# Optimization experiments

Hardware: AMD Instinct MI355X
Metric: run time of the kernel (lower is better)

Reference implementation:

```python
import jax, jax.numpy as jnp
import numpy as np


def setup_inputs() -> dict:
    key = jax.random.key(0)
    k0, k1, k2, k3 = jax.random.split(key, 4)
    B, T, C = 4, 2048, 1024
    x = jax.random.normal(k0, (B, T, C), dtype=jnp.float32)
    s = C ** -0.5  # init-scale for weights so activations stay O(1)
    Wq = jax.random.normal(k1, (C, C), dtype=jnp.float32) * s
    Wk = jax.random.normal(k2, (C, C), dtype=jnp.float32) * s
    Wv = jax.random.normal(k3, (C, C), dtype=jnp.float32) * s
    return {"x": x, "Wq": Wq, "Wk": Wk, "Wv": Wv}


def reference(x, Wq, Wk, Wv):
    B, T, C = x.shape
    # torch nn.Linear: y = x @ W.T
    q = jnp.einsum('btc,dc->btd', x, Wq)
    k = jnp.einsum('btc,dc->btd', x, Wk)
    v = jnp.einsum('btc,dc->btd', x, Wv)
    scale = C ** -0.5
    wei = jnp.einsum('btd,bsd->bts', q, k) * scale  # [B, T, T]
    causal = jnp.tril(jnp.ones((T, T), dtype=bool))
    wei = jnp.where(causal, wei, -jnp.inf)
    wei = jax.nn.softmax(wei, axis=-1)
    out = jnp.einsum('bts,bsd->btd', wei, v)
    return out
```

## Files before the change

### kernel.cpp

```cpp
#include <hip/hip_runtime.h>
#include <hip/hip_bf16.h>
#include <math.h>

#define B_ 4
#define T_ 2048
#define C_ 1024
#define M_ (B_*T_)

typedef __attribute__((ext_vector_type(8))) __bf16 bf16x8;
typedef __attribute__((ext_vector_type(4))) float floatx4;

__device__ inline float bf2f(unsigned short u){
    return __uint_as_float(((unsigned)u) << 16);
}
__device__ inline unsigned short f2bf(float f){
    unsigned u = __float_as_uint(f);
    unsigned r = (u + 0x7fffu + ((u >> 16) & 1u)) >> 16;
    return (unsigned short)r;
}

__device__ inline void llds16(const unsigned short* g, unsigned short* lds){
    __builtin_amdgcn_global_load_lds(
        (const __attribute__((address_space(1))) unsigned int*)g,
        (__attribute__((address_space(3))) unsigned int*)(unsigned int)(uintptr_t)lds,
        16, 0, 0);
}

#define NX_ (M_*C_/4)
#define NW_ (C_*C_/4)
__global__ __launch_bounds__(256) void cast_all(
    const float* __restrict__ x, const float* __restrict__ wq,
    const float* __restrict__ wk, const float* __restrict__ wv,
    unsigned short* __restrict__ xb, unsigned short* __restrict__ wb)
{
    int i = blockIdx.x * 256 + threadIdx.x;
    const float* src; unsigned short* dst; int idx;
    if (i < NX_){ src = x; dst = xb; idx = i; }
    else {
        i -= NX_;
        int w = i / NW_; idx = i - w * NW_;
        src = (w == 0) ? wq : ((w == 1) ? wk : wv);
        dst = wb + (size_t)w * C_ * C_;
    }
    float4 v = ((const float4*)src)[idx];
    ((ushort4*)dst)[idx] = make_ushort4(f2bf(v.x), f2bf(v.y), f2bf(v.z), f2bf(v.w));
}

template<int WM, int WN>
__device__ inline void gemm_core(const unsigned short* __restrict__ A,
                                 const unsigned short* __restrict__ Bm,
                                 int lda, int ldb, int m0, int n0, int kTiles,
                                 unsigned short* As, unsigned short* Bs,
                                 floatx4 (*acc)[WN/16])
{
    const int tid  = threadIdx.x;
    const int lane = tid & 63;
    const int wave = tid >> 6;
    const int wm = (wave >> 1) * WM;
    const int wn = (wave & 1) * WN;
    const int fr = lane & 15;
    const int fq = lane >> 4;
    const int cxor = fr & 7;
    const int sr = lane >> 3;
    const int sc = ((lane & 7) ^ ((lane >> 3) & 7)) * 8;

    const unsigned short* gA = A  + (size_t)(m0 + wave * (WM/2) + sr) * lda + sc;
    const unsigned short* gB = Bm + (size_t)(n0 + wave * (WN/2) + sr) * ldb + sc;
    unsigned short* ldsA = As + wave * (WM/2) * 64;
    unsigned short* ldsB = Bs + wave * (WN/2) * 64;

    for (int kt = 0; kt < kTiles; kt++){
        const int k0 = kt * 64;
        __syncthreads();
        #pragma unroll
        for (int i = 0; i < WM/16; i++)
            llds16(gA + (size_t)(i * 8) * lda + k0, ldsA + i * 8 * 64);
        #pragma unroll
        for (int i = 0; i < WN/16; i++)
            llds16(gB + (size_t)(i * 8) * ldb + k0, ldsB + i * 8 * 64);
        __syncthreads();
        #pragma unroll
        for (int ks = 0; ks < 64; ks += 32){
            const int cpos = (((ks >> 3) + fq) ^ cxor) * 8;
            bf16x8 af[WM/16], bv[WN/16];
            #pragma unroll
            for (int i = 0; i < WM/16; i++)
                af[i] = *(const bf16x8*)(As + (wm + i*16 + fr) * 64 + cpos);
            #pragma unroll
            for (int j = 0; j < WN/16; j++)
                bv[j] = *(const bf16x8*)(Bs + (wn + j*16 + fr) * 64 + cpos);
            #pragma unroll
            for (int i = 0; i < WM/16; i++)
                #pragma unroll
                for (int j = 0; j < WN/16; j++)
                    acc[i][j] = __builtin_amdgcn_mfma_f32_16x16x32_bf16(af[i], bv[j], acc[i][j], 0, 0, 0);
        }
    }
}

__global__ __launch_bounds__(256, 4) void proj_gemm(
    const unsigned short* __restrict__ xb,
    const unsigned short* __restrict__ Wb,
    unsigned short* __restrict__ Qb, unsigned short* __restrict__ Kb,
    unsigned short* __restrict__ Vt)
{
    __shared__ unsigned short As[128 * 64];
    __shared__ unsigned short Bs[128 * 64];
    const int L = blockIdx.x;
    const int k = L & 7, j = L >> 3;
    const int m0 = (k * 8 + (j & 7)) * 128;
    const int n0 = ((j >> 3) & 7) * 128;
    const int z  = j >> 6;
    const unsigned short* W = Wb + (size_t)z * C_ * C_;

    floatx4 acc[4][4];
    #pragma unroll
    for (int i = 0; i < 4; i++)
        #pragma unroll
        for (int jj = 0; jj < 4; jj++) acc[i][jj] = (floatx4){0.f,0.f,0.f,0.f};
    gemm_core<64, 64>(xb, W, C_, C_, m0, n0, C_ / 64, As, Bs, acc);

    const int lane = threadIdx.x & 63, wave = threadIdx.x >> 6;
    const int wm = (wave >> 1) * 64, wn = (wave & 1) * 64;
    const int fr = lane & 15, fq = lane >> 4;

    if (z < 2){
        unsigned short* Y = z ? Kb : Qb;
        #pragma unroll
        for (int i = 0; i < 4; i++)
            #pragma unroll
            for (int jj = 0; jj < 4; jj++)
                #pragma unroll
                for (int r = 0; r < 4; r++){
                    int row = m0 + wm + i*16 + fq*4 + r;
                    int col = n0 + wn + jj*16 + fr;
                    Y[(size_t)row * C_ + col] = f2bf(acc[i][jj][r]);
                }
    } else {
        #pragma unroll
        for (int i = 0; i < 4; i++)
            #pragma unroll
            for (int jj = 0; jj < 4; jj++){
                int row = m0 + wm + i*16 + fq*4;
                int col = n0 + wn + jj*16 + fr;
                int b = row / T_, t = row % T_;
                ushort4 o = make_ushort4(f2bf(acc[i][jj][0]), f2bf(acc[i][jj][1]),
                                         f2bf(acc[i][jj][2]), f2bf(acc[i][jj][3]));
                *(ushort4*)&Vt[(size_t)b * C_ * T_ + (size_t)col * T_ + t] = o;
            }
    }
}

__global__ __launch_bounds__(256, 4) void score_gemm(
    const unsigned short* __restrict__ Qb, const unsigned short* __restrict__ Kb,
    unsigned short* __restrict__ P, float* __restrict__ l)
{
    const int L = blockIdx.x;
    const int k = L & 7, j = L >> 3;
    const int b = j / 17, rr = j % 17;
    int ti, si;
    if (rr <= 15 - k){ ti = 15 - k; si = rr; }
    else             { ti = k;      si = rr - (16 - k); }
    const int t0 = ti * 128, s0 = si * 128;

    __shared__ unsigned short As[128 * 64];
    __shared__ unsigned short Bs[128 * 64];
    floatx4 acc[4][4];
    #pragma unroll
    for (int i = 0; i < 4; i++)
        #pragma unroll
        for (int jj = 0; jj < 4; jj++) acc[i][jj] = (floatx4){0.f,0.f,0.f,0.f};
    gemm_core<64, 64>(Qb + (size_t)b * T_ * C_, Kb + (size_t)b * T_ * C_,
                      C_, C_, t0, s0, C_ / 64, As, Bs, acc);

    const int lane = threadIdx.x & 63, wave = threadIdx.x >> 6;
    const int wm = (wave >> 1) * 64, wn = (wave & 1) * 64;
    const int fr = lane & 15, fq = lane >> 4;
    unsigned short* Pb = P + (size_t)b * T_ * T_;
    const float scale = 0.03125f;
    float rsl[4][4];
    #pragma unroll
    for (int i = 0; i < 4; i++)
        #pragma unroll
        for (int r2 = 0; r2 < 4; r2++) rsl[i][r2] = 0.f;

    #pragma unroll
    for (int i = 0; i < 4; i++)
        #pragma unroll
        for (int jj = 0; jj < 4; jj++)
            #pragma unroll
            for (int r2 = 0; r2 < 4; r2++){
                int t = t0 + wm + i*16 + fq*4 + r2;
                int s = s0 + wn + jj*16 + fr;
                float v = (s <= t) ? __expf(acc[i][jj][r2] * scale) : 0.f;
                rsl[i][r2] += v;
                Pb[(size_t)t * T_ + s] = f2bf(v);
            }
    #pragma unroll
    for (int i = 0; i < 4; i++)
        #pragma unroll
        for (int r2 = 0; r2 < 4; r2++){
            float v = rsl[i][r2];
            v += __shfl_xor(v, 1, 64);
            v += __shfl_xor(v, 2, 64);
            v += __shfl_xor(v, 4, 64);
            v += __shfl_xor(v, 8, 64);
            if (fr == 0){
                int t = t0 + wm + i*16 + fq*4 + r2;
                atomicAdd(&l[(size_t)b * T_ + t], v);
            }
        }
}

__global__ __launch_bounds__(256, 4) void pv_gemm(
    const unsigned short* __restrict__ P, const unsigned short* __restrict__ Vt,
    const float* __restrict__ l, float* __restrict__ out)
{
    const int L = blockIdx.x;
    const int k = L & 7, j = L >> 3;
    const int b = j >> 4;
    const int n0 = (j & 15) * 64;

    __shared__ unsigned short As[128 * 64];
    __shared__ unsigned short Bs[64 * 64];

    const int lane = threadIdx.x & 63, wave = threadIdx.x >> 6;
    const int wm = (wave >> 1) * 64, wn = (wave & 1) * 32;
    const int fr = lane & 15, fq = lane >> 4;
    float* ob = out + (size_t)b * T_ * C_;
    const float* lb = l + (size_t)b * T_;

    #pragma unroll
    for (int phase = 0; phase < 2; phase++){
        const int ti = phase ? k : (15 - k);
        const int t0 = ti * 128;
        const int kTiles = 2 * (ti + 1);

        floatx4 acc[4][2];
        #pragma unroll
        for (int i = 0; i < 4; i++)
            #pragma unroll
            for (int jj = 0; jj < 2; jj++) acc[i][jj] = (floatx4){0.f,0.f,0.f,0.f};
        gemm_core<64, 32>(P + (size_t)b * T_ * T_, Vt + (size_t)b * C_ * T_,
                          T_, T_, t0, n0, kTiles, As, Bs, acc);

        #pragma unroll
        for (int i = 0; i < 4; i++){
            float inv[4];
            #pragma unroll
            for (int r2 = 0; r2 < 4; r2++)
                inv[r2] = 1.f / lb[t0 + wm + i*16 + fq*4 + r2];
            #pragma unroll
            for (int jj = 0; jj < 2; jj++)
                #pragma unroll
                for (int r2 = 0; r2 < 4; r2++){
                    int t = t0 + wm + i*16 + fq*4 + r2;
                    int d = n0 + wn + jj*16 + fr;
                    ob[(size_t)t * C_ + d] = acc[i][jj][r2] * inv[r2];
                }
        }
    }
}

extern "C" void kernel_launch(void* const* d_in, const int* in_sizes, int n_in,
                              void* d_out, int out_size, void* d_ws, size_t ws_size,
                              hipStream_t stream)
{
    const float* x  = (const float*)d_in[0];
    const float* Wq = (const float*)d_in[1];
    const float* Wk = (const float*)d_in[2];
    const float* Wv = (const float*)d_in[3];
    float* out = (float*)d_out;

    unsigned short* Qb = (unsigned short*)d_ws;
    unsigned short* Kb = Qb + (size_t)M_ * C_;
    unsigned short* Vt = Kb + (size_t)M_ * C_;
    unsigned short* P  = Vt + (size_t)M_ * C_;
    float* l = (float*)(P + (size_t)M_ * T_);
    unsigned short* xb = P;
    unsigned short* Wb = P + (size_t)M_ * C_;

    cast_all<<<(NX_ + 3 * NW_ + 255) / 256, 256, 0, stream>>>(x, Wq, Wk, Wv, xb, Wb);
    hipMemsetAsync(l, 0, (size_t)M_ * sizeof(float), stream);
    proj_gemm <<<1536, 256, 0, stream>>>(xb, Wb, Qb, Kb, Vt);
    score_gemm<<<544,  256, 0, stream>>>(Qb, Kb, P, l);
    pv_gemm   <<<512,  256, 0, stream>>>(P, Vt, l, out);
}
```

Baseline: 217.9 us.

## Double-buffer LDS tiles in score and PV GEMMs to overlap loads with MFMA

Adds a double-buffered GEMM core that issues the direct global-to-LDS loads for the next K tile while MFMAs run on the current tile, with one barrier per iteration. The score and PV kernels switch to it, doubling their shared-memory tiles, and their launch bounds drop from 4 to 2 blocks per CU. The aim is to hide global load latency inside each block. The cost is lower occupancy from the larger LDS footprint, and correctness depends on the barrier also waiting for the asynchronous LDS loads to finish.

```diff
diff --git a/kernel.cpp b/kernel.cpp
--- a/kernel.cpp
+++ b/kernel.cpp
@@ -98,6 +98,74 @@
     }
 }
 
+template<int WM, int WN>
+__device__ inline void gemm_core_db(const unsigned short* __restrict__ A,
+                                    const unsigned short* __restrict__ Bm,
+                                    int lda, int ldb, int m0, int n0, int kTiles,
+                                    unsigned short* As, unsigned short* Bs,
+                                    floatx4 (*acc)[WN/16])
+{
+    const int tid  = threadIdx.x;
+    const int lane = tid & 63;
+    const int wave = tid >> 6;
+    const int wm = (wave >> 1) * WM;
+    const int wn = (wave & 1) * WN;
+    const int fr = lane & 15;
+    const int fq = lane >> 4;
+    const int cxor = fr & 7;
+    const int sr = lane >> 3;
+    const int sc = ((lane & 7) ^ ((lane >> 3) & 7)) * 8;
+    const int ASZ = 2 * WM * 64;
+    const int BSZ = 2 * WN * 64;
+
+    const unsigned short* gA = A  + (size_t)(m0 + wave * (WM/2) + sr) * lda + sc;
+    const unsigned short* gB = Bm + (size_t)(n0 + wave * (WN/2) + sr) * ldb + sc;
+    unsigned short* ldsA = As + wave * (WM/2) * 64;
+    unsigned short* ldsB = Bs + wave * (WN/2) * 64;
+
+    __syncthreads();
+    #pragma unroll
+    for (int i = 0; i < WM/16; i++)
+        llds16(gA + (size_t)(i * 8) * lda, ldsA + i * 8 * 64);
+    #pragma unroll
+    for (int i = 0; i < WN/16; i++)
+        llds16(gB + (size_t)(i * 8) * ldb, ldsB + i * 8 * 64);
+
+    for (int kt = 0; kt < kTiles; kt++){
+        const int cur = kt & 1;
+        __syncthreads();
+        if (kt + 1 < kTiles){
+            const int nk0 = (kt + 1) * 64;
+            unsigned short* lA = ldsA + (cur ^ 1) * ASZ;
+            unsigned short* lB = ldsB + (cur ^ 1) * BSZ;
+            #pragma unroll
+            for (int i = 0; i < WM/16; i++)
+                llds16(gA + (size_t)(i * 8) * lda + nk0, lA + i * 8 * 64);
+            #pragma unroll
+            for (int i = 0; i < WN/16; i++)
+                llds16(gB + (size_t)(i * 8) * ldb + nk0, lB + i * 8 * 64);
+        }
+        const unsigned short* rA = As + cur * ASZ;
+        const unsigned short* rB = Bs + cur * BSZ;
+        #pragma unroll
+        for (int ks = 0; ks < 64; ks += 32){
+            const int cpos = (((ks >> 3) + fq) ^ cxor) * 8;
+            bf16x8 af[WM/16], bv[WN/16];
+            #pragma unroll
+            for (int i = 0; i < WM/16; i++)
+                af[i] = *(const bf16x8*)(rA + (wm + i*16 + fr) * 64 + cpos);
+            #pragma unroll
+            for (int j = 0; j < WN/16; j++)
+                bv[j] = *(const bf16x8*)(rB + (wn + j*16 + fr) * 64 + cpos);
+            #pragma unroll
+            for (int i = 0; i < WM/16; i++)
+                #pragma unroll
+                for (int j = 0; j < WN/16; j++)
+                    acc[i][j] = __builtin_amdgcn_mfma_f32_16x16x32_bf16(af[i], bv[j], acc[i][j], 0, 0, 0);
+        }
+    }
+}
+
 __global__ __launch_bounds__(256, 4) void proj_gemm(
     const unsigned short* __restrict__ xb,
     const unsigned short* __restrict__ Wb,
@@ -151,7 +219,7 @@
     }
 }
 
-__global__ __launch_bounds__(256, 4) void score_gemm(
+__global__ __launch_bounds__(256, 2) void score_gemm(
     const unsigned short* __restrict__ Qb, const unsigned short* __restrict__ Kb,
     unsigned short* __restrict__ P, float* __restrict__ l)
 {
@@ -163,15 +231,15 @@
     else             { ti = k;      si = rr - (16 - k); }
     const int t0 = ti * 128, s0 = si * 128;
 
-    __shared__ unsigned short As[128 * 64];
-    __shared__ unsigned short Bs[128 * 64];
+    __shared__ unsigned short As[2 * 128 * 64];
+    __shared__ unsigned short Bs[2 * 128 * 64];
     floatx4 acc[4][4];
     #pragma unroll
     for (int i = 0; i < 4; i++)
         #pragma unroll
         for (int jj = 0; jj < 4; jj++) acc[i][jj] = (floatx4){0.f,0.f,0.f,0.f};
-    gemm_core<64, 64>(Qb + (size_t)b * T_ * C_, Kb + (size_t)b * T_ * C_,
-                      C_, C_, t0, s0, C_ / 64, As, Bs, acc);
+    gemm_core_db<64, 64>(Qb + (size_t)b * T_ * C_, Kb + (size_t)b * T_ * C_,
+                         C_, C_, t0, s0, C_ / 64, As, Bs, acc);
 
     const int lane = threadIdx.x & 63, wave = threadIdx.x >> 6;
     const int wm = (wave >> 1) * 64, wn = (wave & 1) * 64;
@@ -212,7 +280,7 @@
         }
 }
 
-__global__ __launch_bounds__(256, 4) void pv_gemm(
+__global__ __launch_bounds__(256, 2) void pv_gemm(
     const unsigned short* __restrict__ P, const unsigned short* __restrict__ Vt,
     const float* __restrict__ l, float* __restrict__ out)
 {
@@ -221,8 +289,8 @@
     const int b = j >> 4;
     const int n0 = (j & 15) * 64;
 
-    __shared__ unsigned short As[128 * 64];
-    __shared__ unsigned short Bs[64 * 64];
+    __shared__ unsigned short As[2 * 128 * 64];
+    __shared__ unsigned short Bs[2 * 64 * 64];
 
     const int lane = threadIdx.x & 63, wave = threadIdx.x >> 6;
     const int wm = (wave >> 1) * 64, wn = (wave & 1) * 32;
@@ -241,8 +309,8 @@
         for (int i = 0; i < 4; i++)
             #pragma unroll
             for (int jj = 0; jj < 2; jj++) acc[i][jj] = (floatx4){0.f,0.f,0.f,0.f};
-        gemm_core<64, 32>(P + (size_t)b * T_ * T_, Vt + (size_t)b * C_ * T_,
-                          T_, T_, t0, n0, kTiles, As, Bs, acc);
+        gemm_core_db<64, 32>(P + (size_t)b * T_ * T_, Vt + (size_t)b * C_ * T_,
+                             T_, T_, t0, n0, kTiles, As, Bs, acc);
 
         #pragma unroll
         for (int i = 0; i < 4; i++){
```

Result: faster. 211.9 us (-2.7%).
